# Kernel tuning notes

Hardware: AMD Instinct MI355X
Metric: run time of the kernel (lower is better)

The kernel has to match this reference:

```python
import jax, jax.numpy as jnp
import numpy as np
from jax import lax

EPS = 1e-6

def build_hh_matrix(V):
    """V: [d, d] rows are (unnormalized) Householder vectors.
    Returns Q = prod_i (I - 2 v_i v_i^T) applied left-to-right, matching
    the torch loop Q <- Q @ (I - 2 v v^T) == Q - 2 (Q v) v^T (rank-1 update)."""
    d = V.shape[0]
    Vn = V / (jnp.linalg.norm(V, axis=1, keepdims=True) + EPS)
    def step(Q, v):
        Qv = Q @ v                      # [d]
        return Q - 2.0 * jnp.outer(Qv, v), None
    Q, _ = lax.scan(step, jnp.eye(d, dtype=V.dtype), Vn)
    return Q


def setup_inputs() -> dict:
    key = jax.random.key(0)
    k1, k2 = jax.random.split(key)
    x = jax.random.normal(k1, (131072, 512), dtype=jnp.float32)
    hd_vecs = jax.random.normal(k2, (1, 512, 512), dtype=jnp.float32)
    return {"x": x, "hd_vecs": hd_vecs}


def reference(x, hd_vecs):
    # n_mat == 1 branch: out = (Q @ x^T)^T = x @ Q^T
    Q = build_hh_matrix(hd_vecs[0])     # [d, d]
    return x @ Q.T                      # [npatches, d]
```

## Files before the change

kernel.cpp:

```cpp
#include <hip/hip_runtime.h>
#include <hip/hip_bf16.h>
#include <stdint.h>

#define EPS 1e-6f

typedef unsigned short ushort_t;
using frag  = __attribute__((ext_vector_type(8))) short;
using f32x4 = __attribute__((ext_vector_type(4))) float;
using fv4   = __attribute__((ext_vector_type(4))) float;

__device__ __forceinline__ ushort_t f2bf(float f) {
  uint32_t u = __builtin_bit_cast(uint32_t, f);
  u += 0x7FFFu + ((u >> 16) & 1u);
  return (ushort_t)(u >> 16);
}

__device__ __forceinline__ frag cvt8(fv4 lo, fv4 hi) {
  frag v;
  v[0]=(short)f2bf(lo[0]); v[1]=(short)f2bf(lo[1]); v[2]=(short)f2bf(lo[2]); v[3]=(short)f2bf(lo[3]);
  v[4]=(short)f2bf(hi[0]); v[5]=(short)f2bf(hi[1]); v[6]=(short)f2bf(hi[2]); v[7]=(short)f2bf(hi[3]);
  return v;
}

__global__ __launch_bounds__(256) void normalize_kernel(const float* __restrict__ V,
                                                        float* __restrict__ Vn) {
  const int gw   = blockIdx.x * 4 + (threadIdx.x >> 6);
  const int lane = threadIdx.x & 63;
  const float4* src = (const float4*)(V + (size_t)gw * 512) + lane * 2;
  float4 a = src[0], c = src[1];
  float s = a.x*a.x + a.y*a.y + a.z*a.z + a.w*a.w
          + c.x*c.x + c.y*c.y + c.z*c.z + c.w*c.w;
  #pragma unroll
  for (int off = 32; off; off >>= 1) s += __shfl_xor(s, off);
  float inv = 1.f / (sqrtf(s) + EPS);
  float4 na = make_float4(a.x*inv, a.y*inv, a.z*inv, a.w*inv);
  float4 nc = make_float4(c.x*inv, c.y*inv, c.z*inv, c.w*inv);
  float4* dst = (float4*)(Vn + (size_t)gw * 512) + lane * 2;
  dst[0] = na; dst[1] = nc;
}

__global__ __launch_bounds__(256) void gram_kernel(const float* __restrict__ Vn,
                                                   float* __restrict__ G) {
  const int gi = blockIdx.x;
  const int b = gi >> 7, i = gi & 127;
  const int w = threadIdx.x >> 6, lane = threadIdx.x & 63;
  const float4* ri = (const float4*)(Vn + (size_t)gi * 512) + lane * 2;
  float4 a0 = ri[0], a1 = ri[1];
  for (int j = i + 1 + w; j < 128; j += 4) {
    const float4* rj = (const float4*)(Vn + (size_t)(b * 128 + j) * 512) + lane * 2;
    float4 c0 = rj[0], c1 = rj[1];
    float s = a0.x*c0.x + a0.y*c0.y + a0.z*c0.z + a0.w*c0.w
            + a1.x*c1.x + a1.y*c1.y + a1.z*c1.z + a1.w*c1.w;
    #pragma unroll
    for (int off = 32; off; off >>= 1) s += __shfl_xor(s, off);
    if (lane == 0) G[(size_t)gi * 128 + j] = s;
  }
}

__global__ __launch_bounds__(256) void trinv_kernel(float* __restrict__ GT) {
  __shared__ float Gs[128][132];
  __shared__ float Ai[64][68];
  __shared__ float Di[64][68];
  __shared__ float C1[64][68];
  const int b = blockIdx.x, tid = threadIdx.x;
  float* Gg = GT + b * 16384;

  {
    const int r = tid >> 1, h = tid & 1;
    const float4* src = (const float4*)(Gg + r * 128 + h * 64);
    float4* dst = (float4*)(&Gs[r][h * 64]);
    #pragma unroll
    for (int e = 0; e < 16; ++e) dst[e] = src[e];
  }
  __syncthreads();

  const int wave = tid >> 6, lane = tid & 63;
  if (wave < 2) {
    const int o = wave * 64;
    float t[64];
    #pragma unroll
    for (int i = 63; i >= 0; --i) {
      float s = (i == lane) ? 1.f : 0.f;
      #pragma unroll
      for (int j = i + 1; j < 64; ++j) s -= Gs[o + i][o + j] * t[j];
      t[i] = 2.f * s;
    }
    float (*OUT)[68] = wave ? Di : Ai;
    #pragma unroll
    for (int i = 0; i < 64; ++i) OUT[i][lane] = t[i];
  }
  __syncthreads();

  const int i0 = (tid >> 4) << 2;
  const int j0 = (tid & 15) << 2;

  {
    fv4 acc[4] = {};
    for (int l = 0; l < 64; l += 4) {
      fv4 g[4], d[4];
      #pragma unroll
      for (int r = 0; r < 4; ++r) g[r] = *(const fv4*)(&Gs[i0 + r][64 + l]);
      #pragma unroll
      for (int r = 0; r < 4; ++r) d[r] = *(const fv4*)(&Di[l + r][j0]);
      #pragma unroll
      for (int r = 0; r < 4; ++r)
        #pragma unroll
        for (int l2 = 0; l2 < 4; ++l2)
          #pragma unroll
          for (int q = 0; q < 4; ++q)
            acc[r][q] = fmaf(g[r][l2], d[l2][q], acc[r][q]);
    }
    #pragma unroll
    for (int r = 0; r < 4; ++r) *(fv4*)(&C1[i0 + r][j0]) = acc[r];
  }
  __syncthreads();

  {
    fv4 acc[4] = {};
    for (int l = 0; l < 64; l += 4) {
      fv4 g[4], d[4];
      #pragma unroll
      for (int r = 0; r < 4; ++r) g[r] = *(const fv4*)(&Ai[i0 + r][l]);
      #pragma unroll
      for (int r = 0; r < 4; ++r) d[r] = *(const fv4*)(&C1[l + r][j0]);
      #pragma unroll
      for (int r = 0; r < 4; ++r)
        #pragma unroll
        for (int l2 = 0; l2 < 4; ++l2)
          #pragma unroll
          for (int q = 0; q < 4; ++q)
            acc[r][q] = fmaf(g[r][l2], d[l2][q], acc[r][q]);
    }
    #pragma unroll
    for (int r = 0; r < 4; ++r)
      #pragma unroll
      for (int q = 0; q < 4; ++q)
        Gg[(64 + j0 + q) * 128 + (i0 + r)] = -acc[r][q];
  }

  {
    const int j = tid >> 1, h = tid & 1;
    if (j < 64) {
      if (h == 0) { for (int i = 0; i < 64; ++i) Gg[j * 128 + i] = Ai[i][j]; }
      else        { for (int i = 0; i < 64; ++i) Gg[j * 128 + 64 + i] = 0.f; }
    } else if (h == 1) {
      for (int i = 0; i < 64; ++i) Gg[j * 128 + 64 + i] = Di[i][j - 64];
    }
  }
}

__global__ __launch_bounds__(256) void chain_kernel(const float* __restrict__ Vn,
                                                    const float* __restrict__ Tt,
                                                    ushort_t* __restrict__ Qf) {
  __shared__ float Qt[4][512];
  __shared__ float Pp[4][4][64];
  __shared__ float Ps[4][128];
  __shared__ float Asm[4][128];
  const int t = threadIdx.x, w = t >> 6, lane = t & 63;
  const int m0 = blockIdx.x * 4;

  for (int idx = t; idx < 2048; idx += 256) {
    int i = idx >> 9, k = idx & 511;
    Qt[i][k] = (m0 + i == k) ? 1.f : 0.f;
  }

  for (int b = 0; b < 4; ++b) {
    if (b == 0) {
      __syncthreads();
      if (t < 128) {
        #pragma unroll
        for (int i = 0; i < 4; ++i) Ps[i][t] = Vn[t * 512 + m0 + i];
      }
      __syncthreads();
    } else {
      for (int ch = 0; ch < 2; ++ch) {
        __syncthreads();
        const int n = ch * 64 + lane;
        const float* vrow = Vn + (size_t)(b * 128 + n) * 512;
        float pa[4] = {0.f, 0.f, 0.f, 0.f};
        #pragma unroll 8
        for (int k4 = 0; k4 < 32; ++k4) {
          int kk = w * 128 + k4 * 4;
          float4 vv = *(const float4*)(vrow + kk);
          #pragma unroll
          for (int i = 0; i < 4; ++i) {
            float4 qq = *(const float4*)(&Qt[i][kk]);
            pa[i] += qq.x*vv.x + qq.y*vv.y + qq.z*vv.z + qq.w*vv.w;
          }
        }
        #pragma unroll
        for (int i = 0; i < 4; ++i) Pp[w][i][lane] = pa[i];
        __syncthreads();
        if (w < 2) {
          #pragma unroll
          for (int i2 = 0; i2 < 2; ++i2) {
            int i = w * 2 + i2;
            Ps[i][ch * 64 + lane] = Pp[0][i][lane] + Pp[1][i][lane]
                                  + Pp[2][i][lane] + Pp[3][i][lane];
          }
        }
      }
      __syncthreads();
    }
    {
      const float* trow = Tt + b * 16384 + (t >> 1) * 128 + (t & 1) * 64;
      float aa[4] = {0.f, 0.f, 0.f, 0.f};
      #pragma unroll 4
      for (int j4 = 0; j4 < 16; ++j4) {
        float4 tv = *(const float4*)(trow + j4 * 4);
        int j = (t & 1) * 64 + j4 * 4;
        #pragma unroll
        for (int i = 0; i < 4; ++i) {
          float4 pv = *(const float4*)(&Ps[i][j]);
          aa[i] += pv.x*tv.x + pv.y*tv.y + pv.z*tv.z + pv.w*tv.w;
        }
      }
      #pragma unroll
      for (int i = 0; i < 4; ++i) {
        float o = __shfl_xor(aa[i], 1);
        if ((t & 1) == 0) Asm[i][t >> 1] = aa[i] + o;
      }
    }
    __syncthreads();
    {
      float acc0[4] = {0.f,0.f,0.f,0.f}, acc1[4] = {0.f,0.f,0.f,0.f};
      const float* vb = Vn + (size_t)b * 65536 + t * 2;
      #pragma unroll 4
      for (int n = 0; n < 128; ++n) {
        float2 vv = *(const float2*)(vb + (size_t)n * 512);
        #pragma unroll
        for (int i = 0; i < 4; ++i) {
          float a = Asm[i][n];
          acc0[i] = fmaf(a, vv.x, acc0[i]);
          acc1[i] = fmaf(a, vv.y, acc1[i]);
        }
      }
      #pragma unroll
      for (int i = 0; i < 4; ++i) {
        Qt[i][t * 2]     -= acc0[i];
        Qt[i][t * 2 + 1] -= acc1[i];
      }
    }
  }
  __syncthreads();
  {
    int i = t >> 6, ks = (t >> 2) & 15, lg = t & 3;
    int r = m0 + i;
    int nt = r >> 4, l = lg * 16 + (r & 15);
    const float* src = &Qt[i][ks * 32 + lg * 8];
    frag v;
    #pragma unroll
    for (int j = 0; j < 8; ++j) v[j] = (short)f2bf(src[j]);
    *(frag*)(Qf + ((size_t)(ks * 32 + nt) * 64 + l) * 8) = v;
  }
}

__global__ __launch_bounds__(512) void final_gemm(const float* __restrict__ X,
                                                  const ushort_t* __restrict__ Qf,
                                                  float* __restrict__ out) {
  __shared__ __align__(16) char smem[49152];
  const int tid = threadIdx.x;
  const int w = tid >> 6, lane = tid & 63;
  const int m0 = blockIdx.x * 64;

  const int r0 = tid >> 4,          p0 = tid & 15;
  const int r1 = (tid + 512) >> 4,  p1 = tid & 15;
  const int g0 = p0 ^ (((r0 & 7) << 1) | ((r0 >> 3) & 1));
  const int g1 = p1 ^ (((r1 & 7) << 1) | ((r1 >> 3) & 1));
  const float* src0 = X + (size_t)(m0 + r0) * 512 + g0 * 4;
  const float* src1 = X + (size_t)(m0 + r1) * 512 + g1 * 4;
  const int ldsb0 = w * 1024;
  const int ldsb1 = 8192 + w * 1024;

  #define GLOAD(KT, BUF) do { \
    __builtin_amdgcn_global_load_lds( \
      (const __attribute__((address_space(1))) uint32_t*)(src0 + (KT) * 64), \
      (__attribute__((address_space(3))) uint32_t*)(smem + (BUF) * 16384 + ldsb0), 16, 0, 0); \
    __builtin_amdgcn_global_load_lds( \
      (const __attribute__((address_space(1))) uint32_t*)(src1 + (KT) * 64), \
      (__attribute__((address_space(3))) uint32_t*)(smem + (BUF) * 16384 + ldsb1), 16, 0, 0); \
  } while (0)

  const ushort_t* qb = Qf + ((size_t)(w * 4) * 64 + lane) * 8;
  frag bs[3][4];
  #define BLOAD(KS, SLOT) do { \
    _Pragma("unroll") \
    for (int j = 0; j < 4; ++j) \
      bs[SLOT][j] = *(const frag*)(qb + (size_t)(KS) * 16384 + j * 512); \
  } while (0)

  int aoff[4];
  #pragma unroll
  for (int mf = 0; mf < 4; ++mf) {
    int row = mf * 16 + (lane & 15);
    int xm = ((row & 7) << 1) | ((row >> 3) & 1);
    aoff[mf] = row * 256 + ((((lane >> 4) * 2) ^ xm) << 4);
  }

  f32x4 acc[4][4];
  #pragma unroll
  for (int i = 0; i < 4; ++i)
    #pragma unroll
    for (int j = 0; j < 4; ++j) acc[i][j] = (f32x4){0.f, 0.f, 0.f, 0.f};

  GLOAD(0, 0); GLOAD(1, 1); BLOAD(0, 0); BLOAD(1, 1);
  asm volatile("s_waitcnt vmcnt(10)" ::: "memory");
  __builtin_amdgcn_s_barrier();

  #pragma unroll
  for (int kt = 0; kt < 8; ++kt) {
    const char* bb = smem + (kt % 3) * 16384;
    if (kt < 6) GLOAD(kt + 2, (kt + 2) % 3);
    if (kt < 7) BLOAD(2 * kt + 2, (2 * kt + 2) % 3);
    {
      frag a_[4];
      #pragma unroll
      for (int mf = 0; mf < 4; ++mf) {
        fv4 lo = *(const fv4*)(bb + aoff[mf]);
        fv4 hi = *(const fv4*)(bb + (aoff[mf] ^ 16));
        a_[mf] = cvt8(lo, hi);
      }
      #pragma unroll
      for (int mf = 0; mf < 4; ++mf)
        #pragma unroll
        for (int j = 0; j < 4; ++j)
          acc[mf][j] = __builtin_amdgcn_mfma_f32_16x16x32_bf16(a_[mf], bs[(2 * kt) % 3][j], acc[mf][j], 0, 0, 0);
    }
    if (kt < 7) BLOAD(2 * kt + 3, (2 * kt + 3) % 3);
    {
      frag a_[4];
      #pragma unroll
      for (int mf = 0; mf < 4; ++mf) {
        fv4 lo = *(const fv4*)(bb + (aoff[mf] ^ 128));
        fv4 hi = *(const fv4*)(bb + (aoff[mf] ^ 128 ^ 16));
        a_[mf] = cvt8(lo, hi);
      }
      #pragma unroll
      for (int mf = 0; mf < 4; ++mf)
        #pragma unroll
        for (int j = 0; j < 4; ++j)
          acc[mf][j] = __builtin_amdgcn_mfma_f32_16x16x32_bf16(a_[mf], bs[(2 * kt + 1) % 3][j], acc[mf][j], 0, 0, 0);
    }
    asm volatile("s_waitcnt vmcnt(10)" ::: "memory");
    __builtin_amdgcn_s_barrier();
  }

  float (*Ep)[516] = (float (*)[516])smem;
  #pragma unroll
  for (int mf = 0; mf < 4; ++mf) {
    __builtin_amdgcn_s_barrier();
    #pragma unroll
    for (int j = 0; j < 4; ++j) {
      int col = w * 64 + j * 16 + (lane & 15);
      #pragma unroll
      for (int r = 0; r < 4; ++r)
        Ep[((lane >> 4) << 2) + r][col] = acc[mf][j][r];
    }
    asm volatile("s_waitcnt lgkmcnt(0)" ::: "memory");
    __builtin_amdgcn_s_barrier();
    #pragma unroll
    for (int e = 0; e < 4; ++e) {
      int idx = e * 512 + tid;
      int rr = idx >> 7, c4 = idx & 127;
      float4 v = *(const float4*)(&Ep[rr][c4 * 4]);
      *(float4*)(out + (size_t)(m0 + mf * 16 + rr) * 512 + c4 * 4) = v;
    }
  }
  #undef GLOAD
  #undef BLOAD
}

extern "C" void kernel_launch(void* const* d_in, const int* in_sizes, int n_in,
                              void* d_out, int out_size, void* d_ws, size_t ws_size,
                              hipStream_t stream) {
  const float* x = (const float*)d_in[0];
  const float* V = (const float*)d_in[1];
  float* out = (float*)d_out;
  float* ws  = (float*)d_ws;

  float*    Vn = ws;
  float*    GT = ws + 262144;
  ushort_t* Qf = (ushort_t*)(ws + 327680);

  normalize_kernel<<<128, 256, 0, stream>>>(V, Vn);
  gram_kernel<<<512, 256, 0, stream>>>(Vn, GT);
  trinv_kernel<<<4, 256, 0, stream>>>(GT);
  chain_kernel<<<128, 256, 0, stream>>>(Vn, GT, Qf);
  final_gemm<<<2048, 512, 0, stream>>>(x, Qf, out);
}
```

Baseline: 288.3 us.

## Replace triple-buffered X pipeline with two half-row bursts into larger LDS

The final GEMM used to stream X through a three-stage ring of 64-column LDS tiles with a barrier every k-step. It now loads half of each 64-row block (256 columns) into a 64KB LDS buffer in one burst, computes four k-steps with no barriers, then waits and loads the second half. Per-iteration barriers go away and launch bounds request 4 blocks per CU. The cost is that the load of the second half no longer overlaps with compute, and the larger LDS footprint may limit occupancy.

```diff
diff --git a/kernel.cpp b/kernel.cpp
--- a/kernel.cpp
+++ b/kernel.cpp
@@ -255,30 +255,25 @@
   }
 }
 
-__global__ __launch_bounds__(512) void final_gemm(const float* __restrict__ X,
-                                                  const ushort_t* __restrict__ Qf,
-                                                  float* __restrict__ out) {
-  __shared__ __align__(16) char smem[49152];
+__global__ __launch_bounds__(512, 4) void final_gemm(const float* __restrict__ X,
+                                                     const ushort_t* __restrict__ Qf,
+                                                     float* __restrict__ out) {
+  __shared__ __align__(16) char smem[65536];
   const int tid = threadIdx.x;
   const int w = tid >> 6, lane = tid & 63;
   const int m0 = blockIdx.x * 64;
-
-  const int r0 = tid >> 4,          p0 = tid & 15;
-  const int r1 = (tid + 512) >> 4,  p1 = tid & 15;
-  const int g0 = p0 ^ (((r0 & 7) << 1) | ((r0 >> 3) & 1));
-  const int g1 = p1 ^ (((r1 & 7) << 1) | ((r1 >> 3) & 1));
-  const float* src0 = X + (size_t)(m0 + r0) * 512 + g0 * 4;
-  const float* src1 = X + (size_t)(m0 + r1) * 512 + g1 * 4;
-  const int ldsb0 = w * 1024;
-  const int ldsb1 = 8192 + w * 1024;
-
-  #define GLOAD(KT, BUF) do { \
-    __builtin_amdgcn_global_load_lds( \
-      (const __attribute__((address_space(1))) uint32_t*)(src0 + (KT) * 64), \
-      (__attribute__((address_space(3))) uint32_t*)(smem + (BUF) * 16384 + ldsb0), 16, 0, 0); \
-    __builtin_amdgcn_global_load_lds( \
-      (const __attribute__((address_space(1))) uint32_t*)(src1 + (KT) * 64), \
-      (__attribute__((address_space(3))) uint32_t*)(smem + (BUF) * 16384 + ldsb1), 16, 0, 0); \
+  const int lane2 = lane ^ (w & 1);
+
+  #define GBURST(P) do { \
+    _Pragma("unroll") \
+    for (int i = 0; i < 8; ++i) { \
+      const float* s_ = X + (size_t)(m0 + w * 8 + i) * 512 + (P) * 256 \
+                        + ((lane2 ^ (i << 1)) << 2); \
+      __builtin_amdgcn_global_load_lds( \
+        (const __attribute__((address_space(1))) uint32_t*)s_, \
+        (__attribute__((address_space(3))) uint32_t*)(smem + (w * 8 + i) * 1024), \
+        16, 0, 0); \
+    } \
   } while (0)
 
   const ushort_t* qb = Qf + ((size_t)(w * 4) * 64 + lane) * 8;
@@ -289,12 +284,12 @@
       bs[SLOT][j] = *(const frag*)(qb + (size_t)(KS) * 16384 + j * 512); \
   } while (0)
 
-  int aoff[4];
+  int a0[4];
   #pragma unroll
   for (int mf = 0; mf < 4; ++mf) {
-    int row = mf * 16 + (lane & 15);
-    int xm = ((row & 7) << 1) | ((row >> 3) & 1);
-    aoff[mf] = row * 256 + ((((lane >> 4) * 2) ^ xm) << 4);
+    int r = mf * 16 + (lane & 15);
+    int xm = ((r & 7) << 1) | ((r >> 3) & 1);
+    a0[mf] = r * 1024 + (((((lane >> 4) * 2)) ^ xm) << 4);
   }
 
   f32x4 acc[4][4];
@@ -303,21 +298,30 @@
     #pragma unroll
     for (int j = 0; j < 4; ++j) acc[i][j] = (f32x4){0.f, 0.f, 0.f, 0.f};
 
-  GLOAD(0, 0); GLOAD(1, 1); BLOAD(0, 0); BLOAD(1, 1);
-  asm volatile("s_waitcnt vmcnt(10)" ::: "memory");
+  GBURST(0); BLOAD(0, 0); BLOAD(1, 1);
+  asm volatile("s_waitcnt vmcnt(8)" ::: "memory");
   __builtin_amdgcn_s_barrier();
+  __builtin_amdgcn_sched_barrier(0);
 
   #pragma unroll
   for (int kt = 0; kt < 8; ++kt) {
-    const char* bb = smem + (kt % 3) * 16384;
-    if (kt < 6) GLOAD(kt + 2, (kt + 2) % 3);
+    if (kt == 4) {
+      __builtin_amdgcn_s_barrier();
+      __builtin_amdgcn_sched_barrier(0);
+      GBURST(1);
+      asm volatile("s_waitcnt vmcnt(0)" ::: "memory");
+      __builtin_amdgcn_s_barrier();
+      __builtin_amdgcn_sched_barrier(0);
+    }
+    const int ktl = kt & 3;
     if (kt < 7) BLOAD(2 * kt + 2, (2 * kt + 2) % 3);
     {
       frag a_[4];
       #pragma unroll
       for (int mf = 0; mf < 4; ++mf) {
-        fv4 lo = *(const fv4*)(bb + aoff[mf]);
-        fv4 hi = *(const fv4*)(bb + (aoff[mf] ^ 16));
+        int off = a0[mf] + ktl * 256;
+        fv4 lo = *(const fv4*)(smem + off);
+        fv4 hi = *(const fv4*)(smem + (off ^ 16));
         a_[mf] = cvt8(lo, hi);
       }
       #pragma unroll
@@ -331,8 +335,9 @@
       frag a_[4];
       #pragma unroll
       for (int mf = 0; mf < 4; ++mf) {
-        fv4 lo = *(const fv4*)(bb + (aoff[mf] ^ 128));
-        fv4 hi = *(const fv4*)(bb + (aoff[mf] ^ 128 ^ 16));
+        int off = (a0[mf] + ktl * 256) ^ 128;
+        fv4 lo = *(const fv4*)(smem + off);
+        fv4 hi = *(const fv4*)(smem + (off ^ 16));
         a_[mf] = cvt8(lo, hi);
       }
       #pragma unroll
@@ -341,14 +346,13 @@
         for (int j = 0; j < 4; ++j)
           acc[mf][j] = __builtin_amdgcn_mfma_f32_16x16x32_bf16(a_[mf], bs[(2 * kt + 1) % 3][j], acc[mf][j], 0, 0, 0);
     }
-    asm volatile("s_waitcnt vmcnt(10)" ::: "memory");
-    __builtin_amdgcn_s_barrier();
   }
 
   float (*Ep)[516] = (float (*)[516])smem;
   #pragma unroll
   for (int mf = 0; mf < 4; ++mf) {
     __builtin_amdgcn_s_barrier();
+    __builtin_amdgcn_sched_barrier(0);
     #pragma unroll
     for (int j = 0; j < 4; ++j) {
       int col = w * 64 + j * 16 + (lane & 15);
@@ -358,6 +362,7 @@
     }
     asm volatile("s_waitcnt lgkmcnt(0)" ::: "memory");
     __builtin_amdgcn_s_barrier();
+    __builtin_amdgcn_sched_barrier(0);
     #pragma unroll
     for (int e = 0; e < 4; ++e) {
       int idx = e * 512 + tid;
@@ -366,7 +371,7 @@
       *(float4*)(out + (size_t)(m0 + mf * 16 + rr) * 512 + c4 * 4) = v;
     }
   }
-  #undef GLOAD
+  #undef GBURST
   #undef BLOAD
 }
 
```

Result: slower. 375.3 us (+30.2%).
